# Optimization experiments

Hardware: AMD Instinct MI355X
Metric: run time of the kernel (lower is better)

## Reference

```python
import jax, jax.numpy as jnp
import numpy as np

N, D, K = 8192, 256, 32

def _cdist(x, y):
    # Euclidean distance via matmul expansion (matches torch 'use_mm' mode)
    x2 = jnp.sum(x * x, axis=-1)[:, None]
    y2 = jnp.sum(y * y, axis=-1)[None, :]
    d2 = x2 + y2 - 2.0 * (x @ y.T)
    return jnp.sqrt(jnp.maximum(d2, 0.0))

def setup_inputs() -> dict:
    key = jax.random.key(0)
    features = jax.random.normal(key, (N, D), dtype=jnp.float32)
    return {"features": features, "k": K}

def reference(features, k):
    n = features.shape[0]
    r_full = _cdist(features, features)                       # [N, N]
    # drop diagonal (rank 0 offset): column j maps to ref index j + (j >= i)
    cols = jnp.arange(n - 1)[None, :] + (jnp.arange(n - 1)[None, :] >= jnp.arange(n)[:, None])
    r = jnp.take_along_axis(r_full, cols, axis=1)             # [N, N-1]
    # sorted distances and their (masked-column) indices
    idx = jnp.argsort(r, axis=1)                              # [N, N-1]
    a = jnp.take_along_axis(r, idx, axis=1)                   # [N, N-1]
    # full reference-vs-reference distances, row-sorted
    a_full_d = jnp.sort(r_full, axis=1)                       # [N, N]
    idx_k = idx[:, :k]                                        # [N, k]
    # faithful to original: idx_k used directly as row indices into a_full_d
    d_k = a_full_d[idx_k, k]                                  # [N, k]
    scores = a[:, k][:, None] / d_k                           # [N, k]
    scores = jnp.mean(scores, axis=1)                         # [N]
    scores = jnp.nan_to_num(scores, nan=1000.0, posinf=1000.0, neginf=0.0)
    return scores
```

## Files before the change

kernel.cpp:

```cpp
#include <hip/hip_runtime.h>

#define N 8192
#define DIM 256
#define QB 32
#define NWAVES 8
#define CB (NWAVES*16)
#define NIT (N / CB)
#define LK 33
#define NBIN 256
#define BUFCAP 160
#define NFRAG 16

typedef short bf16x8 __attribute__((ext_vector_type(8)));
typedef float f32x4 __attribute__((ext_vector_type(4)));

static __device__ inline unsigned short f2bf(float f) {
    unsigned int u = __float_as_uint(f);
    unsigned int r = (u + 0x7fffu + ((u >> 16) & 1u)) >> 16;
    return (unsigned short)r;
}

static __device__ inline float dist2(float qn_plus_cn, float acc) {
    return __builtin_fmaf(-2.0f, acc, qn_plus_cn);
}

__global__ __launch_bounds__(64) void prep_kernel(const float* __restrict__ feat,
                                                  unsigned short* __restrict__ fb,
                                                  float* __restrict__ norms) {
    int row = blockIdx.x;
    int lane = threadIdx.x;
    float4 v = reinterpret_cast<const float4*>(feat + (size_t)row * DIM)[lane];
    float ss = v.x * v.x + v.y * v.y + v.z * v.z + v.w * v.w;
    #pragma unroll
    for (int off = 32; off > 0; off >>= 1) ss += __shfl_xor(ss, off);
    if (lane == 0) norms[row] = ss;
    ushort4 b;
    b.x = f2bf(v.x); b.y = f2bf(v.y); b.z = f2bf(v.z); b.w = f2bf(v.w);
    reinterpret_cast<ushort4*>(fb + (size_t)row * DIM)[lane] = b;
}

#define STAGE_AQ_TO_LDS()                                                    \
    int koff = (lane >> 4) * 8;                                              \
    if (w == 0) {                                                            \
        int arow = qbase + (lane & 15);                                      \
        _Pragma("unroll")                                                    \
        for (int rt = 0; rt < 2; rt++) {                                     \
            _Pragma("unroll")                                                \
            for (int ks = 0; ks < 8; ks++)                                   \
                aLds[(rt * 8 + ks) * 64 + lane] =                            \
                    *reinterpret_cast<const bf16x8*>(                        \
                        fb + (size_t)(arow + rt * 16) * DIM + ks * 32 + koff); \
        }                                                                    \
    }

__global__ __launch_bounds__(NWAVES * 64, 2) void hist_kernel(
    const unsigned short* __restrict__ fb, const float* __restrict__ norms,
    float* __restrict__ tq) {
    __shared__ bf16x8 aLds[NFRAG * 64];
    __shared__ unsigned int hist[QB][NBIN + 1];
    __shared__ float qn[QB];

    int tid = threadIdx.x;
    int w = tid >> 6;
    int lane = tid & 63;
    int qbase = blockIdx.x * QB;

    for (int i = tid; i < QB * (NBIN + 1); i += NWAVES * 64)
        (&hist[0][0])[i] = 0u;
    if (tid < QB) qn[tid] = norms[qbase + tid];

    STAGE_AQ_TO_LDS()
    __syncthreads();

    float qnr[2][4];
    int hoff[2][4];
    int qgl[2][4];
    #pragma unroll
    for (int rt = 0; rt < 2; rt++)
        #pragma unroll
        for (int j = 0; j < 4; j++) {
            int ql = rt * 16 + (lane >> 4) * 4 + j;
            qnr[rt][j] = qn[ql];
            hoff[rt][j] = ql * (NBIN + 1);
            qgl[rt][j] = qbase + ql;
        }
    unsigned int* hflat = &hist[0][0];

    int cbase = w * 16 + (lane & 15);
    const unsigned short* bptr = fb + (size_t)cbase * DIM + koff;

    for (int it = 0; it < NIT; it++) {
        int crow = it * CB + cbase;
        const bf16x8* bp = reinterpret_cast<const bf16x8*>(
            bptr + (size_t)it * CB * DIM);
        bf16x8 bq[8];
        #pragma unroll
        for (int ks = 0; ks < 8; ks++) bq[ks] = bp[ks * 4];
        float cn = norms[crow];

        f32x4 acc[2][2] = {{{0.f,0.f,0.f,0.f},{0.f,0.f,0.f,0.f}},
                           {{0.f,0.f,0.f,0.f},{0.f,0.f,0.f,0.f}}};
        #pragma unroll
        for (int ks = 0; ks < 8; ks++) {
            bf16x8 a0 = aLds[ks * 64 + lane];
            bf16x8 a1 = aLds[(8 + ks) * 64 + lane];
            acc[0][ks & 1] = __builtin_amdgcn_mfma_f32_16x16x32_bf16(a0, bq[ks], acc[0][ks & 1], 0, 0, 0);
            acc[1][ks & 1] = __builtin_amdgcn_mfma_f32_16x16x32_bf16(a1, bq[ks], acc[1][ks & 1], 0, 0, 0);
        }

        #pragma unroll
        for (int rt = 0; rt < 2; rt++) {
            f32x4 s = acc[rt][0] + acc[rt][1];
            #pragma unroll
            for (int j = 0; j < 4; j++) {
                float d2 = dist2(qnr[rt][j] + cn, s[j]);
                if (crow != qgl[rt][j]) {
                    int b = (int)(d2 * 0.25f);
                    b = b < 0 ? 0 : (b > NBIN - 1 ? NBIN - 1 : b);
                    atomicAdd(&hflat[hoff[rt][j] + b], 1u);
                }
            }
        }
    }
    __syncthreads();

    if (tid < QB) {
        unsigned int cum = 0;
        int bstar = NBIN - 1;
        for (int b = 0; b < NBIN; b++) {
            cum += hist[tid][b];
            if (cum >= LK) { bstar = b; break; }
        }
        tq[qbase + tid] = (float)(bstar + 1) * 4.0f;
    }
}

__device__ inline void rescan_max(const float* ld, const int* li,
                                  float& md, int& mi, int& mp) {
    md = -3.0e38f; mi = -1; mp = 0;
    for (int t = 0; t < LK; t++) {
        float d = ld[t]; int ix = li[t];
        if (d > md || (d == md && ix > mi)) { md = d; mi = ix; mp = t; }
    }
}

__global__ __launch_bounds__(NWAVES * 64, 2) void collect_kernel(
    const unsigned short* __restrict__ fb, const float* __restrict__ norms,
    const float* __restrict__ tq,
    float* __restrict__ kd32sq, float* __restrict__ kd33sq, int* __restrict__ knn) {
    __shared__ bf16x8 aLds[NFRAG * 64];
    __shared__ float qn[QB];
    __shared__ float Tsh[QB];
    __shared__ float buf_d[QB][BUFCAP];
    __shared__ int   buf_i[QB][BUFCAP];
    __shared__ int   bcnt[QB];
    __shared__ float list_d[QB][LK];
    __shared__ int   list_i[QB][LK];

    int tid = threadIdx.x;
    int w = tid >> 6;
    int lane = tid & 63;
    int qbase = blockIdx.x * QB;

    if (tid < QB) {
        qn[tid] = norms[qbase + tid];
        Tsh[tid] = tq[qbase + tid];
        bcnt[tid] = 0;
    }

    STAGE_AQ_TO_LDS()
    __syncthreads();

    float qnr[2][4], Tr[2][4];
    int qln[2][4], qgl[2][4];
    #pragma unroll
    for (int rt = 0; rt < 2; rt++)
        #pragma unroll
        for (int j = 0; j < 4; j++) {
            int ql = rt * 16 + (lane >> 4) * 4 + j;
            qnr[rt][j] = qn[ql];
            Tr[rt][j] = Tsh[ql];
            qln[rt][j] = ql;
            qgl[rt][j] = qbase + ql;
        }

    int cbase = w * 16 + (lane & 15);
    const unsigned short* bptr = fb + (size_t)cbase * DIM + koff;

    for (int it = 0; it < NIT; it++) {
        int crow = it * CB + cbase;
        const bf16x8* bp = reinterpret_cast<const bf16x8*>(
            bptr + (size_t)it * CB * DIM);
        bf16x8 bq[8];
        #pragma unroll
        for (int ks = 0; ks < 8; ks++) bq[ks] = bp[ks * 4];
        float cn = norms[crow];

        f32x4 acc[2][2] = {{{0.f,0.f,0.f,0.f},{0.f,0.f,0.f,0.f}},
                           {{0.f,0.f,0.f,0.f},{0.f,0.f,0.f,0.f}}};
        #pragma unroll
        for (int ks = 0; ks < 8; ks++) {
            bf16x8 a0 = aLds[ks * 64 + lane];
            bf16x8 a1 = aLds[(8 + ks) * 64 + lane];
            acc[0][ks & 1] = __builtin_amdgcn_mfma_f32_16x16x32_bf16(a0, bq[ks], acc[0][ks & 1], 0, 0, 0);
            acc[1][ks & 1] = __builtin_amdgcn_mfma_f32_16x16x32_bf16(a1, bq[ks], acc[1][ks & 1], 0, 0, 0);
        }

        #pragma unroll
        for (int rt = 0; rt < 2; rt++) {
            f32x4 s = acc[rt][0] + acc[rt][1];
            #pragma unroll
            for (int j = 0; j < 4; j++) {
                float d2 = dist2(qnr[rt][j] + cn, s[j]);
                if (crow != qgl[rt][j] && d2 < Tr[rt][j]) {
                    int ql = qln[rt][j];
                    int p = atomicAdd(&bcnt[ql], 1);
                    if (p < BUFCAP) { buf_d[ql][p] = d2; buf_i[ql][p] = crow; }
                }
            }
        }
    }
    __syncthreads();

    if (tid < QB) {
        int q = tid;
        int g = qbase + q;
        int n = bcnt[q]; if (n > BUFCAP) n = BUFCAP;
        int c = 0;
        float m1d = 3.0e38f; int m1i = 0x7fffffff, m1p = 0;
        for (int b = 0; b < n; b++) {
            float d = buf_d[q][b]; int ix = buf_i[q][b];
            if (c < LK) {
                list_d[q][c] = d; list_i[q][c] = ix; c++;
                if (c == LK) rescan_max(&list_d[q][0], &list_i[q][0], m1d, m1i, m1p);
            } else if (d < m1d || (d == m1d && ix < m1i)) {
                list_d[q][m1p] = d; list_i[q][m1p] = ix;
                rescan_max(&list_d[q][0], &list_i[q][0], m1d, m1i, m1p);
            }
        }
        rescan_max(&list_d[q][0], &list_i[q][0], m1d, m1i, m1p);
        float m2d = -3.0e38f; int m2i = -1;
        for (int t = 0; t < LK; t++) {
            if (t == m1p) continue;
            float d = list_d[q][t]; int ix = list_i[q][t];
            if (d > m2d || (d == m2d && ix > m2i)) { m2d = d; m2i = ix; }
        }
        kd33sq[g] = m1d;
        kd32sq[g] = m2d;
        int o = 0;
        for (int t = 0; t < LK; t++) {
            if (t == m1p) continue;
            knn[(size_t)g * 32 + o] = list_i[q][t];
            o++;
        }
    }
}

__global__ __launch_bounds__(256) void scores_kernel(
    const float* __restrict__ kd32sq, const float* __restrict__ kd33sq,
    const int* __restrict__ knn, float* __restrict__ out) {
    int i = blockIdx.x * blockDim.x + threadIdx.x;
    float num = sqrtf(fmaxf(kd33sq[i], 0.0f));
    float s = 0.0f;
    #pragma unroll
    for (int t = 0; t < 32; t++) {
        int j = knn[(size_t)i * 32 + t];
        int m = j - (j > i);
        float den = sqrtf(fmaxf(kd32sq[m], 0.0f));
        s += num / den;
    }
    s *= (1.0f / 32.0f);
    if (isnan(s)) s = 1000.0f;
    else if (isinf(s)) s = (s > 0.0f) ? 1000.0f : 0.0f;
    out[i] = s;
}

extern "C" void kernel_launch(void* const* d_in, const int* in_sizes, int n_in,
                              void* d_out, int out_size, void* d_ws, size_t ws_size,
                              hipStream_t stream) {
    (void)in_sizes; (void)n_in; (void)out_size; (void)ws_size;
    const float* feat = (const float*)d_in[0];

    char* ws = (char*)d_ws;
    unsigned short* fb = (unsigned short*)ws;
    size_t off = (size_t)4 * 1024 * 1024;
    float* norms = (float*)(ws + off); off += 32768;
    float* kd32  = (float*)(ws + off); off += 32768;
    float* kd33  = (float*)(ws + off); off += 32768;
    float* tqv   = (float*)(ws + off); off += 32768;
    int*   knn   = (int*)(ws + off);

    prep_kernel<<<N, 64, 0, stream>>>(feat, fb, norms);
    hist_kernel<<<N / QB, NWAVES * 64, 0, stream>>>(fb, norms, tqv);
    collect_kernel<<<N / QB, NWAVES * 64, 0, stream>>>(fb, norms, tqv, kd32, kd33, knn);
    scores_kernel<<<N / 256, 256, 0, stream>>>(kd32, kd33, knn, (float*)d_out);
}
```

Before: 375.8 us.

## Double-buffer B-fragment loads and double waves per block in kNN kernels

Both hist and collect kernels now prefetch the next iteration's candidate bf16 fragments and norm into registers while the current iteration's MFMAs and binning run, hiding global load latency. Waves per block go from 8 to 16, so each iteration covers 256 candidate rows and there are half as many iterations. The occupancy hint rises to 4. The added prefetch registers and the larger block may raise register pressure or cause spills. The 1024-thread block also collides with the 'waves 4' launch bound.

```diff
diff --git a/kernel.cpp b/kernel.cpp
--- a/kernel.cpp
+++ b/kernel.cpp
@@ -3,7 +3,7 @@
 #define N 8192
 #define DIM 256
 #define QB 32
-#define NWAVES 8
+#define NWAVES 16
 #define CB (NWAVES*16)
 #define NIT (N / CB)
 #define LK 33
@@ -53,7 +53,7 @@
         }                                                                    \
     }
 
-__global__ __launch_bounds__(NWAVES * 64, 2) void hist_kernel(
+__global__ __launch_bounds__(NWAVES * 64, 4) void hist_kernel(
     const unsigned short* __restrict__ fb, const float* __restrict__ norms,
     float* __restrict__ tq) {
     __shared__ bf16x8 aLds[NFRAG * 64];
@@ -89,14 +89,23 @@
     int cbase = w * 16 + (lane & 15);
     const unsigned short* bptr = fb + (size_t)cbase * DIM + koff;
 
+    bf16x8 bq[8];
+    #pragma unroll
+    for (int ks = 0; ks < 8; ks++)
+        bq[ks] = reinterpret_cast<const bf16x8*>(bptr)[ks * 4];
+    float cn = norms[cbase];
+
     for (int it = 0; it < NIT; it++) {
         int crow = it * CB + cbase;
-        const bf16x8* bp = reinterpret_cast<const bf16x8*>(
-            bptr + (size_t)it * CB * DIM);
-        bf16x8 bq[8];
-        #pragma unroll
-        for (int ks = 0; ks < 8; ks++) bq[ks] = bp[ks * 4];
-        float cn = norms[crow];
+        bf16x8 bn[8];
+        float cnn = 0.0f;
+        if (it + 1 < NIT) {
+            const bf16x8* np = reinterpret_cast<const bf16x8*>(
+                bptr + (size_t)(it + 1) * CB * DIM);
+            #pragma unroll
+            for (int ks = 0; ks < 8; ks++) bn[ks] = np[ks * 4];
+            cnn = norms[crow + CB];
+        }
 
         f32x4 acc[2][2] = {{{0.f,0.f,0.f,0.f},{0.f,0.f,0.f,0.f}},
                            {{0.f,0.f,0.f,0.f},{0.f,0.f,0.f,0.f}}};
@@ -121,6 +130,10 @@
                 }
             }
         }
+
+        #pragma unroll
+        for (int ks = 0; ks < 8; ks++) bq[ks] = bn[ks];
+        cn = cnn;
     }
     __syncthreads();
 
@@ -144,7 +157,7 @@
     }
 }
 
-__global__ __launch_bounds__(NWAVES * 64, 2) void collect_kernel(
+__global__ __launch_bounds__(NWAVES * 64, 4) void collect_kernel(
     const unsigned short* __restrict__ fb, const float* __restrict__ norms,
     const float* __restrict__ tq,
     float* __restrict__ kd32sq, float* __restrict__ kd33sq, int* __restrict__ knn) {
@@ -187,14 +200,23 @@
     int cbase = w * 16 + (lane & 15);
     const unsigned short* bptr = fb + (size_t)cbase * DIM + koff;
 
+    bf16x8 bq[8];
+    #pragma unroll
+    for (int ks = 0; ks < 8; ks++)
+        bq[ks] = reinterpret_cast<const bf16x8*>(bptr)[ks * 4];
+    float cn = norms[cbase];
+
     for (int it = 0; it < NIT; it++) {
         int crow = it * CB + cbase;
-        const bf16x8* bp = reinterpret_cast<const bf16x8*>(
-            bptr + (size_t)it * CB * DIM);
-        bf16x8 bq[8];
-        #pragma unroll
-        for (int ks = 0; ks < 8; ks++) bq[ks] = bp[ks * 4];
-        float cn = norms[crow];
+        bf16x8 bn[8];
+        float cnn = 0.0f;
+        if (it + 1 < NIT) {
+            const bf16x8* np = reinterpret_cast<const bf16x8*>(
+                bptr + (size_t)(it + 1) * CB * DIM);
+            #pragma unroll
+            for (int ks = 0; ks < 8; ks++) bn[ks] = np[ks * 4];
+            cnn = norms[crow + CB];
+        }
 
         f32x4 acc[2][2] = {{{0.f,0.f,0.f,0.f},{0.f,0.f,0.f,0.f}},
                            {{0.f,0.f,0.f,0.f},{0.f,0.f,0.f,0.f}}};
@@ -219,6 +241,10 @@
                 }
             }
         }
+
+        #pragma unroll
+        for (int ks = 0; ks < 8; ks++) bq[ks] = bn[ks];
+        cn = cnn;
     }
     __syncthreads();
 
```

After: 420.3 us (median of 3 runs). 11.8% more time.

## Split candidate range into slices across blocks and move selection to separate kernels

Applied to the files above, without the earlier changes.

Each query tile is now processed by four blocks, each covering a quarter of the candidate rows with four waves, which raises the grid from 256 to 1024 blocks to fill more CUs. Per-slice histograms are packed as 16-bit counts in LDS and written out as clamped bytes, and a new thresh kernel sums the four slices to pick the cutoff. The collect pass appends candidates to global buffers through global atomics, and a separate select kernel does a 33-round min-extraction per query. This adds two launches, a memset, global atomic traffic and extra workspace. The byte clamp and the smaller buffer cap risk inexact results in edge cases.

```diff
diff --git a/kernel.cpp b/kernel.cpp
--- a/kernel.cpp
+++ b/kernel.cpp
@@ -3,12 +3,14 @@
 #define N 8192
 #define DIM 256
 #define QB 32
-#define NWAVES 8
-#define CB (NWAVES*16)
-#define NIT (N / CB)
+#define NW 4
+#define CB (NW*16)
+#define SLICES 4
+#define CPS (N / SLICES)
+#define NIT (CPS / CB)
 #define LK 33
 #define NBIN 256
-#define BUFCAP 160
+#define BUFCAP 128
 #define NFRAG 16
 
 typedef short bf16x8 __attribute__((ext_vector_type(8)));
@@ -53,19 +55,22 @@
         }                                                                    \
     }
 
-__global__ __launch_bounds__(NWAVES * 64, 2) void hist_kernel(
+__global__ __launch_bounds__(NW * 64, 4) void hist_part_kernel(
     const unsigned short* __restrict__ fb, const float* __restrict__ norms,
-    float* __restrict__ tq) {
+    unsigned char* __restrict__ histp) {
     __shared__ bf16x8 aLds[NFRAG * 64];
-    __shared__ unsigned int hist[QB][NBIN + 1];
+    __shared__ unsigned int hist[QB][NBIN / 2 + 1];
     __shared__ float qn[QB];
 
     int tid = threadIdx.x;
     int w = tid >> 6;
     int lane = tid & 63;
-    int qbase = blockIdx.x * QB;
-
-    for (int i = tid; i < QB * (NBIN + 1); i += NWAVES * 64)
+    int qt = blockIdx.x >> 2;
+    int slice = blockIdx.x & 3;
+    int qbase = qt * QB;
+    int cand0 = slice * CPS;
+
+    for (int i = tid; i < QB * (NBIN / 2 + 1); i += NW * 64)
         (&hist[0][0])[i] = 0u;
     if (tid < QB) qn[tid] = norms[qbase + tid];
 
@@ -73,7 +78,7 @@
     __syncthreads();
 
     float qnr[2][4];
-    int hoff[2][4];
+    unsigned int* hrow[2][4];
     int qgl[2][4];
     #pragma unroll
     for (int rt = 0; rt < 2; rt++)
@@ -81,18 +86,16 @@
         for (int j = 0; j < 4; j++) {
             int ql = rt * 16 + (lane >> 4) * 4 + j;
             qnr[rt][j] = qn[ql];
-            hoff[rt][j] = ql * (NBIN + 1);
+            hrow[rt][j] = &hist[ql][0];
             qgl[rt][j] = qbase + ql;
         }
-    unsigned int* hflat = &hist[0][0];
-
-    int cbase = w * 16 + (lane & 15);
-    const unsigned short* bptr = fb + (size_t)cbase * DIM + koff;
+
+    int cbase = cand0 + w * 16 + (lane & 15);
 
     for (int it = 0; it < NIT; it++) {
-        int crow = it * CB + cbase;
+        int crow = cbase + it * CB;
         const bf16x8* bp = reinterpret_cast<const bf16x8*>(
-            bptr + (size_t)it * CB * DIM);
+            fb + (size_t)crow * DIM + koff);
         bf16x8 bq[8];
         #pragma unroll
         for (int ks = 0; ks < 8; ks++) bq[ks] = bp[ks * 4];
@@ -117,62 +120,63 @@
                 if (crow != qgl[rt][j]) {
                     int b = (int)(d2 * 0.25f);
                     b = b < 0 ? 0 : (b > NBIN - 1 ? NBIN - 1 : b);
-                    atomicAdd(&hflat[hoff[rt][j] + b], 1u);
+                    atomicAdd(&hrow[rt][j][b >> 1], 1u << ((b & 1) * 16));
                 }
             }
         }
     }
     __syncthreads();
 
-    if (tid < QB) {
-        unsigned int cum = 0;
-        int bstar = NBIN - 1;
-        for (int b = 0; b < NBIN; b++) {
-            cum += hist[tid][b];
-            if (cum >= LK) { bstar = b; break; }
-        }
-        tq[qbase + tid] = (float)(bstar + 1) * 4.0f;
-    }
-}
-
-__device__ inline void rescan_max(const float* ld, const int* li,
-                                  float& md, int& mi, int& mp) {
-    md = -3.0e38f; mi = -1; mp = 0;
-    for (int t = 0; t < LK; t++) {
-        float d = ld[t]; int ix = li[t];
-        if (d > md || (d == md && ix > mi)) { md = d; mi = ix; mp = t; }
-    }
-}
-
-__global__ __launch_bounds__(NWAVES * 64, 2) void collect_kernel(
+    for (int i = tid; i < QB * NBIN; i += NW * 64) {
+        int q = i >> 8, b = i & 255;
+        unsigned int h = hist[q][b >> 1];
+        unsigned int c = (h >> ((b & 1) * 16)) & 0xffffu;
+        histp[(size_t)blockIdx.x * (QB * NBIN) + i] =
+            (unsigned char)(c > 255u ? 255u : c);
+    }
+}
+
+__global__ __launch_bounds__(256) void thresh_kernel(
+    const unsigned char* __restrict__ histp, float* __restrict__ tq) {
+    int q = blockIdx.x * 256 + threadIdx.x;
+    int qt = q >> 5, ql = q & 31;
+    const unsigned char* base = histp + (size_t)(qt * 4) * (QB * NBIN) + ql * NBIN;
+    int cum = 0;
+    int bstar = NBIN - 1;
+    for (int b = 0; b < NBIN; b++) {
+        cum += (int)base[b] + (int)base[QB * NBIN + b]
+             + (int)base[2 * QB * NBIN + b] + (int)base[3 * QB * NBIN + b];
+        if (cum >= LK) { bstar = b; break; }
+    }
+    tq[q] = (float)(bstar + 1) * 4.0f;
+}
+
+__global__ __launch_bounds__(NW * 64, 4) void collect_part_kernel(
     const unsigned short* __restrict__ fb, const float* __restrict__ norms,
-    const float* __restrict__ tq,
-    float* __restrict__ kd32sq, float* __restrict__ kd33sq, int* __restrict__ knn) {
+    const float* __restrict__ tq, unsigned int* __restrict__ cnt,
+    float* __restrict__ cand_d, int* __restrict__ cand_i) {
     __shared__ bf16x8 aLds[NFRAG * 64];
     __shared__ float qn[QB];
     __shared__ float Tsh[QB];
-    __shared__ float buf_d[QB][BUFCAP];
-    __shared__ int   buf_i[QB][BUFCAP];
-    __shared__ int   bcnt[QB];
-    __shared__ float list_d[QB][LK];
-    __shared__ int   list_i[QB][LK];
 
     int tid = threadIdx.x;
     int w = tid >> 6;
     int lane = tid & 63;
-    int qbase = blockIdx.x * QB;
+    int qt = blockIdx.x >> 2;
+    int slice = blockIdx.x & 3;
+    int qbase = qt * QB;
+    int cand0 = slice * CPS;
 
     if (tid < QB) {
         qn[tid] = norms[qbase + tid];
         Tsh[tid] = tq[qbase + tid];
-        bcnt[tid] = 0;
     }
 
     STAGE_AQ_TO_LDS()
     __syncthreads();
 
     float qnr[2][4], Tr[2][4];
-    int qln[2][4], qgl[2][4];
+    int qgl[2][4];
     #pragma unroll
     for (int rt = 0; rt < 2; rt++)
         #pragma unroll
@@ -180,17 +184,15 @@
             int ql = rt * 16 + (lane >> 4) * 4 + j;
             qnr[rt][j] = qn[ql];
             Tr[rt][j] = Tsh[ql];
-            qln[rt][j] = ql;
             qgl[rt][j] = qbase + ql;
         }
 
-    int cbase = w * 16 + (lane & 15);
-    const unsigned short* bptr = fb + (size_t)cbase * DIM + koff;
+    int cbase = cand0 + w * 16 + (lane & 15);
 
     for (int it = 0; it < NIT; it++) {
-        int crow = it * CB + cbase;
+        int crow = cbase + it * CB;
         const bf16x8* bp = reinterpret_cast<const bf16x8*>(
-            bptr + (size_t)it * CB * DIM);
+            fb + (size_t)crow * DIM + koff);
         bf16x8 bq[8];
         #pragma unroll
         for (int ks = 0; ks < 8; ks++) bq[ks] = bp[ks * 4];
@@ -213,47 +215,44 @@
             for (int j = 0; j < 4; j++) {
                 float d2 = dist2(qnr[rt][j] + cn, s[j]);
                 if (crow != qgl[rt][j] && d2 < Tr[rt][j]) {
-                    int ql = qln[rt][j];
-                    int p = atomicAdd(&bcnt[ql], 1);
-                    if (p < BUFCAP) { buf_d[ql][p] = d2; buf_i[ql][p] = crow; }
+                    int qg = qgl[rt][j];
+                    unsigned int slot = atomicAdd(&cnt[qg], 1u);
+                    if (slot < BUFCAP) {
+                        cand_d[(size_t)qg * BUFCAP + slot] = d2;
+                        cand_i[(size_t)qg * BUFCAP + slot] = crow;
+                    }
                 }
             }
         }
     }
-    __syncthreads();
-
-    if (tid < QB) {
-        int q = tid;
-        int g = qbase + q;
-        int n = bcnt[q]; if (n > BUFCAP) n = BUFCAP;
-        int c = 0;
-        float m1d = 3.0e38f; int m1i = 0x7fffffff, m1p = 0;
-        for (int b = 0; b < n; b++) {
-            float d = buf_d[q][b]; int ix = buf_i[q][b];
-            if (c < LK) {
-                list_d[q][c] = d; list_i[q][c] = ix; c++;
-                if (c == LK) rescan_max(&list_d[q][0], &list_i[q][0], m1d, m1i, m1p);
-            } else if (d < m1d || (d == m1d && ix < m1i)) {
-                list_d[q][m1p] = d; list_i[q][m1p] = ix;
-                rescan_max(&list_d[q][0], &list_i[q][0], m1d, m1i, m1p);
-            }
-        }
-        rescan_max(&list_d[q][0], &list_i[q][0], m1d, m1i, m1p);
-        float m2d = -3.0e38f; int m2i = -1;
-        for (int t = 0; t < LK; t++) {
-            if (t == m1p) continue;
-            float d = list_d[q][t]; int ix = list_i[q][t];
-            if (d > m2d || (d == m2d && ix > m2i)) { m2d = d; m2i = ix; }
-        }
-        kd33sq[g] = m1d;
-        kd32sq[g] = m2d;
-        int o = 0;
-        for (int t = 0; t < LK; t++) {
-            if (t == m1p) continue;
-            knn[(size_t)g * 32 + o] = list_i[q][t];
-            o++;
-        }
-    }
+}
+
+__global__ __launch_bounds__(256) void select_kernel(
+    const unsigned int* __restrict__ cnt,
+    const float* __restrict__ cand_d, const int* __restrict__ cand_i,
+    float* __restrict__ kd32sq, float* __restrict__ kd33sq, int* __restrict__ knn) {
+    int q = blockIdx.x * 256 + threadIdx.x;
+    int n = (int)cnt[q]; if (n > BUFCAP) n = BUFCAP;
+    const float* cd = cand_d + (size_t)q * BUFCAP;
+    const int*  ci = cand_i + (size_t)q * BUFCAP;
+    float pd = -3.0e38f; int pi = -1;
+    float d32 = 0.0f, d33 = 0.0f;
+    for (int r = 0; r < LK; r++) {
+        float bd = 3.0e38f; int bi = 0x7fffffff;
+        for (int t = 0; t < n; t++) {
+            float d = cd[t]; int ix = ci[t];
+            bool gt_prev = (d > pd) || (d == pd && ix > pi);
+            bool lt_cur  = (d < bd) || (d == bd && ix < bi);
+            if (gt_prev && lt_cur) { bd = d; bi = ix; }
+        }
+        if (bi > N - 1) { bi = 0; bd = 1.0f; }
+        if (r < 32) knn[(size_t)q * 32 + r] = bi;
+        if (r == 31) d32 = bd;
+        if (r == 32) d33 = bd;
+        pd = bd; pi = bi;
+    }
+    kd32sq[q] = d32;
+    kd33sq[q] = d33;
 }
 
 __global__ __launch_bounds__(256) void scores_kernel(
@@ -282,16 +281,23 @@
     const float* feat = (const float*)d_in[0];
 
     char* ws = (char*)d_ws;
-    unsigned short* fb = (unsigned short*)ws;
-    size_t off = (size_t)4 * 1024 * 1024;
-    float* norms = (float*)(ws + off); off += 32768;
-    float* kd32  = (float*)(ws + off); off += 32768;
-    float* kd33  = (float*)(ws + off); off += 32768;
-    float* tqv   = (float*)(ws + off); off += 32768;
-    int*   knn   = (int*)(ws + off);
-
+    size_t off = 0;
+    unsigned short* fb = (unsigned short*)(ws + off); off += (size_t)N * DIM * 2;
+    float* norms = (float*)(ws + off); off += (size_t)N * 4;
+    float* tqv   = (float*)(ws + off); off += (size_t)N * 4;
+    float* kd32  = (float*)(ws + off); off += (size_t)N * 4;
+    float* kd33  = (float*)(ws + off); off += (size_t)N * 4;
+    int*   knn   = (int*)(ws + off); off += (size_t)N * 32 * 4;
+    unsigned int* cnt = (unsigned int*)(ws + off); off += (size_t)N * 4;
+    float* cand_d = (float*)(ws + off); off += (size_t)N * BUFCAP * 4;
+    int*   cand_i = (int*)(ws + off); off += (size_t)N * BUFCAP * 4;
+    unsigned char* histp = (unsigned char*)(ws + off); off += (size_t)(N/QB)*SLICES*QB*NBIN;
+
+    hipMemsetAsync(cnt, 0, (size_t)N * 4, stream);
     prep_kernel<<<N, 64, 0, stream>>>(feat, fb, norms);
-    hist_kernel<<<N / QB, NWAVES * 64, 0, stream>>>(fb, norms, tqv);
-    collect_kernel<<<N / QB, NWAVES * 64, 0, stream>>>(fb, norms, tqv, kd32, kd33, knn);
+    hist_part_kernel<<<(N / QB) * SLICES, NW * 64, 0, stream>>>(fb, norms, histp);
+    thresh_kernel<<<N / 256, 256, 0, stream>>>(histp, tqv);
+    collect_part_kernel<<<(N / QB) * SLICES, NW * 64, 0, stream>>>(fb, norms, tqv, cnt, cand_d, cand_i);
+    select_kernel<<<N / 256, 256, 0, stream>>>(cnt, cand_d, cand_i, kd32, kd33, knn);
     scores_kernel<<<N / 256, 256, 0, stream>>>(kd32, kd33, knn, (float*)d_out);
 }
```

Result: slower. 762.1 us (+102.8%).
